# Optimization experiments

Measured on AMD Instinct MI355X. Metric: run time of the kernel, lower is better.

Reference implementation:

```python
import jax, jax.numpy as jnp
import numpy as np

BS, T, F, H, YIN = 32, 64, 32, 256, 10


def setup_inputs() -> dict:
    key = jax.random.key(0)
    ks = jax.random.split(key, 20)
    s = 0.1
    rn = lambda k, shape: jax.random.normal(k, shape, dtype=jnp.float32) * s
    return {
        'Y': jax.random.normal(ks[0], (BS, T, YIN), dtype=jnp.float32),
        'X_p': jax.random.normal(ks[1], (BS, T, F), dtype=jnp.float32),
        'X_n': jax.random.normal(ks[2], (BS, T, F), dtype=jnp.float32),
        # Y-stream LSTM (input 10)
        'Wy': rn(ks[3], (YIN, 4 * H)), 'Uy': rn(ks[4], (H, 4 * H)), 'by': jnp.zeros((4 * H,), jnp.float32),
        # per-feature single-input LSTM banks (F independent LSTMs, input size 1)
        'Wxp': rn(ks[5], (F, 4 * H)), 'Uxp': rn(ks[6], (F, H, 4 * H)), 'bxp': jnp.zeros((F, 4 * H), jnp.float32),
        'Wxn': rn(ks[7], (F, 4 * H)), 'Uxn': rn(ks[8], (F, H, 4 * H)), 'bxn': jnp.zeros((F, 4 * H), jnp.float32),
        # MI-LSTM: main stream gates (i,f,g,o), aux streams (gate, candidate) each
        'Wm': rn(ks[9], (H, 4 * H)), 'Um': rn(ks[10], (H, 4 * H)), 'bm': jnp.zeros((4 * H,), jnp.float32),
        'Wpa': rn(ks[11], (H, 2 * H)), 'Upa': rn(ks[12], (H, 2 * H)), 'bpa': jnp.zeros((2 * H,), jnp.float32),
        'Wna': rn(ks[13], (H, 2 * H)), 'Una': rn(ks[14], (H, 2 * H)), 'bna': jnp.zeros((2 * H,), jnp.float32),
        'Wa': rn(ks[15], (H, H)), 'ba': jnp.zeros((H,), jnp.float32),
        # temporal attention + output head
        'Watt': rn(ks[16], (H, H)), 'batt': jnp.zeros((H,), jnp.float32), 'vatt': rn(ks[17], (H,)),
        'Wlin': rn(ks[18], (H, 1)), 'blin': jnp.zeros((1,), jnp.float32),
    }


def _lstm(x, W, U, b):
    # standard LSTM; x: [bs,T,in] -> hidden sequence [bs,T,H]
    xg = jnp.einsum('bti,ig->btg', x, W) + b  # precompute input projections
    bs, h = x.shape[0], U.shape[0]

    def step(carry, g_t):
        hh, cc = carry
        g = g_t + hh @ U
        i, f, gg, o = jnp.split(g, 4, axis=-1)
        i, f, o = jax.nn.sigmoid(i), jax.nn.sigmoid(f), jax.nn.sigmoid(o)
        cc = f * cc + i * jnp.tanh(gg)
        hh = o * jnp.tanh(cc)
        return (hh, cc), hh

    init = (jnp.zeros((bs, h), x.dtype), jnp.zeros((bs, h), x.dtype))
    _, hs = jax.lax.scan(step, init, jnp.swapaxes(xg, 0, 1))
    return jnp.swapaxes(hs, 0, 1)


def _feature_lstms(x, W, U, b):
    # F independent input-size-1 LSTMs batched into one scan; returns the mean
    # over features of their hidden sequences (= torch.mean(torch.stack(...),0)).
    # x: [bs,T,F], W: [F,4H], U: [F,H,4H], b: [F,4H] -> [bs,T,H]
    xg = x[..., None] * W + b  # [bs,T,F,4H]
    bs, f, h = x.shape[0], W.shape[0], U.shape[1]

    def step(carry, g_t):
        hh, cc = carry  # [bs,F,H]
        g = g_t + jnp.einsum('bfh,fhg->bfg', hh, U)
        i, fg, gg, o = jnp.split(g, 4, axis=-1)
        i, fg, o = jax.nn.sigmoid(i), jax.nn.sigmoid(fg), jax.nn.sigmoid(o)
        cc = fg * cc + i * jnp.tanh(gg)
        hh = o * jnp.tanh(cc)
        return (hh, cc), jnp.mean(hh, axis=1)  # mean over feature-LSTMs

    init = (jnp.zeros((bs, f, h), x.dtype), jnp.zeros((bs, f, h), x.dtype))
    _, hs = jax.lax.scan(step, init, jnp.swapaxes(xg, 0, 1))
    return jnp.swapaxes(hs, 0, 1)


def _milstm(y, p, n, Wm, Um, bm, Wpa, Upa, bpa, Wna, Una, bna, Wa, ba):
    # Multi-input LSTM: main stream y with full i/f/g/o gates; aux streams p,n
    # contribute gated candidates; cell-state attention mixes the 3 candidates.
    yg = jnp.einsum('bth,hg->btg', y, Wm) + bm
    pg = jnp.einsum('bth,hg->btg', p, Wpa) + bpa
    ng = jnp.einsum('bth,hg->btg', n, Wna) + bna
    bs, h = y.shape[0], Um.shape[0]

    def step(carry, gs):
        hh, cc = carry
        yg_t, pg_t, ng_t = gs
        g = yg_t + hh @ Um
        i, f, gy, o = jnp.split(g, 4, axis=-1)
        i, f, o = jax.nn.sigmoid(i), jax.nn.sigmoid(f), jax.nn.sigmoid(o)
        gp = pg_t + hh @ Upa
        ip, cp = jnp.split(gp, 2, axis=-1)
        gn = ng_t + hh @ Una
        inn, cn = jnp.split(gn, 2, axis=-1)
        l = jnp.stack([i * jnp.tanh(gy),
                       jax.nn.sigmoid(ip) * jnp.tanh(cp),
                       jax.nn.sigmoid(inn) * jnp.tanh(cn)], axis=1)  # [bs,3,H]
        att = jnp.tanh(cc @ Wa + ba)  # [bs,H]
        alpha = jax.nn.softmax(jnp.einsum('bkh,bh->bk', l, att), axis=-1)
        ltilde = jnp.einsum('bk,bkh->bh', alpha, l)
        cc = f * cc + ltilde
        hh = o * jnp.tanh(cc)
        return (hh, cc), hh

    init = (jnp.zeros((bs, h), y.dtype), jnp.zeros((bs, h), y.dtype))
    xs = (jnp.swapaxes(yg, 0, 1), jnp.swapaxes(pg, 0, 1), jnp.swapaxes(ng, 0, 1))
    _, hs = jax.lax.scan(step, init, xs)
    return jnp.swapaxes(hs, 0, 1)


def reference(Y, X_p, X_n, Wy, Uy, by, Wxp, Uxp, bxp, Wxn, Uxn, bxn,
              Wm, Um, bm, Wpa, Upa, bpa, Wna, Una, bna, Wa, ba,
              Watt, batt, vatt, Wlin, blin):
    Yh = _lstm(Y, Wy, Uy, by)                      # Y_tilde_hidden [bs,T,H]
    Ph = _feature_lstms(X_p, Wxp, Uxp, bxp)        # P_tilde [bs,T,H]
    Nh = _feature_lstms(X_n, Wxn, Uxn, bxn)        # N_tilde [bs,T,H]
    Hm = _milstm(Yh, Ph, Nh, Wm, Um, bm, Wpa, Upa, bpa, Wna, Una, bna, Wa, ba)
    # temporal additive attention
    s = jnp.einsum('bth,h->bt', jnp.tanh(jnp.einsum('bth,hg->btg', Hm, Watt) + batt), vatt)
    alpha = jax.nn.softmax(s, axis=-1)
    ytilde = jnp.einsum('bt,bth->bh', alpha, Hm)
    return jax.nn.relu(ytilde @ Wlin + blin)       # [bs,1]
```

## Files before the change

kernel.cpp:

```cpp
#include <hip/hip_runtime.h>
#include <math.h>

#define BS 32
#define T 64
#define F 32
#define H 256
#define G4 1024
#define YIN 10

typedef _Float16 f16;
typedef _Float16 f16x8 __attribute__((ext_vector_type(8)));
typedef float f32x4 __attribute__((ext_vector_type(4)));

__device__ __forceinline__ float sigm(float x) { return 1.f / (1.f + expf(-x)); }

__global__ __launch_bounds__(512) void k_prep_u(
    const float* __restrict__ Uxp, const float* __restrict__ Uxn,
    const float* __restrict__ Uy, f16* __restrict__ Uf)
{
  const int slot = blockIdx.x;
  const float* src = (slot < 32) ? (Uxp + (size_t)slot * 262144)
                   : (slot < 64) ? (Uxn + (size_t)(slot - 32) * 262144)
                   : Uy;
  f16* dst = Uf + (size_t)slot * 262144;
  const int lane = threadIdx.x & 63;
  const int kt   = threadIdx.x >> 6;
  const int cl = lane & 15, lq = lane >> 4;
  for (int w = 0; w < 8; ++w)
    for (int nt = 0; nt < 8; ++nt) {
      const int g   = nt >> 1;
      const int col = g * 256 + w * 32 + (nt & 1) * 16 + cl;
      const int k0  = kt * 32 + lq * 8;
      f16x8 v;
      #pragma unroll
      for (int e = 0; e < 8; ++e) v[e] = (f16)src[(size_t)(k0 + e) * G4 + col];
      *(f16x8*)(dst + ((size_t)((w * 8 + nt) * 8 + kt) * 64 + lane) * 8) = v;
    }
}

__global__ __launch_bounds__(1024) void k_prep_w(
    const float* __restrict__ Um, const float* __restrict__ Upa,
    const float* __restrict__ Una, const float* __restrict__ Wa,
    f16* __restrict__ Umh, f16* __restrict__ Uph, f16* __restrict__ Unh,
    f16* __restrict__ Wah)
{
  const int i = blockIdx.x * 1024 + threadIdx.x;
  Umh[i] = (f16)Um[i];
  if (i < 131072) { Uph[i] = (f16)Upa[i]; Unh[i] = (f16)Una[i]; }
  if (i < 65536)  Wah[i] = (f16)Wa[i];
}

__global__ __launch_bounds__(1024) void k_prep_yg0(
    const float* __restrict__ Y, const float* __restrict__ Wy,
    const float* __restrict__ by, float* __restrict__ yg0)
{
  const int col = threadIdx.x;
  const int r0  = blockIdx.x * 16;
  float wv[YIN];
  #pragma unroll
  for (int i = 0; i < YIN; ++i) wv[i] = Wy[i * G4 + col];
  const float bv = by[col];
  for (int r = r0; r < r0 + 16; ++r) {
    float a = bv;
    #pragma unroll
    for (int i = 0; i < YIN; ++i) a += Y[r * YIN + i] * wv[i];
    yg0[(size_t)r * G4 + col] = a;
  }
}

__global__ __launch_bounds__(512, 1) void k_scan(
    const float* __restrict__ Xp, const float* __restrict__ Xn,
    const float* __restrict__ Wxp, const float* __restrict__ bxp,
    const float* __restrict__ Wxn, const float* __restrict__ bxn,
    const f16*  __restrict__ Uf,  const float* __restrict__ yg0,
    float* __restrict__ Yh, float* __restrict__ Ph, float* __restrict__ Nh)
{
  __shared__ __align__(16) f16 hfrag[8 * 64 * 8];
  const int tid = threadIdx.x;
  const int w = tid >> 6, l = tid & 63;
  const int cl = l & 15, lq = l >> 4;
  const int bid = blockIdx.x;
  const bool isY = (bid >= 128);
  int s = 0, f = 0, bh, slot;
  if (isY) { bh = bid & 1; slot = 64; }
  else { s = bid >> 6; f = (bid >> 1) & 31; bh = bid & 1; slot = s * 32 + f; }

  f16x8 U[8][8];
  {
    const f16* ub = Uf + (size_t)slot * 262144 + (size_t)w * 32768 + (size_t)l * 8;
    #pragma unroll
    for (int nt = 0; nt < 8; ++nt)
      #pragma unroll
      for (int kt = 0; kt < 8; ++kt)
        U[nt][kt] = *(const f16x8*)(ub + (nt * 8 + kt) * 512);
  }

  float Wc[4][2], Bc[4][2];
  const float* Xsrc = nullptr;
  if (!isY) {
    const float* Wf = (s ? Wxn : Wxp) + (size_t)f * G4;
    const float* bf = (s ? bxn : bxp) + (size_t)f * G4;
    #pragma unroll
    for (int g = 0; g < 4; ++g)
      #pragma unroll
      for (int q = 0; q < 2; ++q) {
        const int col = g * 256 + w * 32 + q * 16 + cl;
        Wc[g][q] = Wf[col]; Bc[g][q] = bf[col];
      }
    Xsrc = s ? Xn : Xp;
  }
  float* Acc = s ? Nh : Ph;

  float c[2][4];
  #pragma unroll
  for (int q = 0; q < 2; ++q)
    #pragma unroll
    for (int j = 0; j < 4; ++j) c[q][j] = 0.f;

  *(uint4*)(hfrag + tid * 8) = uint4{0, 0, 0, 0};
  __syncthreads();

  for (int t = 0; t < T; ++t) {
    f16x8 a8[8];
    #pragma unroll
    for (int kt = 0; kt < 8; ++kt)
      a8[kt] = *(const f16x8*)(hfrag + kt * 512 + l * 8);

    f32x4 acc[8];
    #pragma unroll
    for (int nt = 0; nt < 8; ++nt) acc[nt] = f32x4{0.f, 0.f, 0.f, 0.f};
    #pragma unroll
    for (int kt = 0; kt < 8; ++kt)
      #pragma unroll
      for (int nt = 0; nt < 8; ++nt)
        acc[nt] = __builtin_amdgcn_mfma_f32_16x16x32_f16(a8[kt], U[nt][kt], acc[nt], 0, 0, 0);

    float xin[4];
    if (!isY) {
      #pragma unroll
      for (int j = 0; j < 4; ++j)
        xin[j] = Xsrc[((size_t)(bh * 16 + lq * 4 + j) * T + t) * F + f];
    }
    __syncthreads();

    #pragma unroll
    for (int q = 0; q < 2; ++q) {
      const int ncol = w * 32 + q * 16 + cl;
      #pragma unroll
      for (int j = 0; j < 4; ++j) {
        const int b = bh * 16 + lq * 4 + j;
        float ip, fp, gp, op;
        if (isY) {
          const float* yrow = yg0 + ((size_t)b * T + t) * G4;
          ip = acc[0 + q][j] + yrow[0 * 256 + ncol];
          fp = acc[2 + q][j] + yrow[1 * 256 + ncol];
          gp = acc[4 + q][j] + yrow[2 * 256 + ncol];
          op = acc[6 + q][j] + yrow[3 * 256 + ncol];
        } else {
          ip = acc[0 + q][j] + xin[j] * Wc[0][q] + Bc[0][q];
          fp = acc[2 + q][j] + xin[j] * Wc[1][q] + Bc[1][q];
          gp = acc[4 + q][j] + xin[j] * Wc[2][q] + Bc[2][q];
          op = acc[6 + q][j] + xin[j] * Wc[3][q] + Bc[3][q];
        }
        const float ig = sigm(ip), fg = sigm(fp), gy = tanhf(gp), og = sigm(op);
        c[q][j] = fg * c[q][j] + ig * gy;
        const float h = og * tanhf(c[q][j]);
        const int dlane = (lq * 4 + j) + (q * 2 + (cl >> 3)) * 16;
        hfrag[w * 512 + dlane * 8 + (cl & 7)] = (f16)h;
        const size_t oidx = ((size_t)b * T + t) * H + ncol;
        if (isY) Yh[oidx] = h;
        else atomicAdd(&Acc[oidx], h * 0.03125f);
      }
    }
    __syncthreads();
  }
}

__global__ __launch_bounds__(1024) void k_xg(
    const float* __restrict__ Yh, const float* __restrict__ Ph, const float* __restrict__ Nh,
    const float* __restrict__ Wm, const float* __restrict__ bm,
    const float* __restrict__ Wpa, const float* __restrict__ bpa,
    const float* __restrict__ Wna, const float* __restrict__ bna,
    float* __restrict__ yg, float* __restrict__ pg, float* __restrict__ ng)
{
  __shared__ __align__(16) float A[8][768];
  const int tid = threadIdx.x;
  const int ro  = blockIdx.x * 8;

  for (int idx = tid; idx < 8 * 768; idx += 1024) {
    const int r = idx / 768, cc = idx % 768;
    const int row = ro + r;
    float v;
    if (cc < 256)      v = Yh[(size_t)row * H + cc];
    else if (cc < 512) v = Ph[(size_t)row * H + (cc - 256)];
    else               v = Nh[(size_t)row * H + (cc - 512)];
    A[r][cc] = v;
  }
  __syncthreads();

  float acc[8];
  #pragma unroll
  for (int r = 0; r < 8; ++r) acc[r] = bm[tid];
  for (int k = 0; k < H; k += 4) {
    const float w0 = Wm[(k + 0) * G4 + tid];
    const float w1 = Wm[(k + 1) * G4 + tid];
    const float w2 = Wm[(k + 2) * G4 + tid];
    const float w3 = Wm[(k + 3) * G4 + tid];
    #pragma unroll
    for (int r = 0; r < 8; ++r) {
      const float4 av = *(const float4*)&A[r][k];
      acc[r] += w0 * av.x + w1 * av.y + w2 * av.z + w3 * av.w;
    }
  }
  #pragma unroll
  for (int r = 0; r < 8; ++r) yg[(size_t)(ro + r) * G4 + tid] = acc[r];

  const int col = tid & 511;
  const float* Wx = (tid < 512) ? Wpa : Wna;
  const float* bx = (tid < 512) ? bpa : bna;
  float* outp     = (tid < 512) ? pg : ng;
  const int aoff  = (tid < 512) ? 256 : 512;
  #pragma unroll
  for (int r = 0; r < 8; ++r) acc[r] = bx[col];
  for (int k = 0; k < H; k += 4) {
    const float w0 = Wx[(k + 0) * 512 + col];
    const float w1 = Wx[(k + 1) * 512 + col];
    const float w2 = Wx[(k + 2) * 512 + col];
    const float w3 = Wx[(k + 3) * 512 + col];
    #pragma unroll
    for (int r = 0; r < 8; ++r) {
      const float4 av = *(const float4*)&A[r][aoff + k];
      acc[r] += w0 * av.x + w1 * av.y + w2 * av.z + w3 * av.w;
    }
  }
  #pragma unroll
  for (int r = 0; r < 8; ++r) outp[(size_t)(ro + r) * 512 + col] = acc[r];
}

__global__ __launch_bounds__(1024) void k_mi(
    const float* __restrict__ yg, const float* __restrict__ pg, const float* __restrict__ ng,
    const f16* __restrict__ Um, const f16* __restrict__ Upa, const f16* __restrict__ Una,
    const f16* __restrict__ Wa, const float* __restrict__ ba,
    float* __restrict__ Hm)
{
  __shared__ __align__(16) float h_lds[H];
  __shared__ __align__(16) float c_lds[H];
  __shared__ float g_lds[G4];
  __shared__ float ga_lds[G4];
  __shared__ float att_lds[H];
  __shared__ float red[3][4];
  const int tid = threadIdx.x;
  const int b   = blockIdx.x;

  if (tid < H) { h_lds[tid] = 0.f; c_lds[tid] = 0.f; }
  __syncthreads();

  for (int t = 0; t < T; ++t) {
    const size_t row = (size_t)b * T + t;

    float gacc = yg[row * G4 + tid];
    for (int k = 0; k < H; k += 4) {
      const float4 hv = *(const float4*)&h_lds[k];
      gacc += (float)Um[(k + 0) * G4 + tid] * hv.x + (float)Um[(k + 1) * G4 + tid] * hv.y
            + (float)Um[(k + 2) * G4 + tid] * hv.z + (float)Um[(k + 3) * G4 + tid] * hv.w;
    }

    const int acol = tid & 511;
    const f16* Ux = (tid < 512) ? Upa : Una;
    float aacc = (tid < 512) ? pg[row * 512 + acol] : ng[row * 512 + acol];
    for (int k = 0; k < H; k += 4) {
      const float4 hv = *(const float4*)&h_lds[k];
      aacc += (float)Ux[(k + 0) * 512 + acol] * hv.x + (float)Ux[(k + 1) * 512 + acol] * hv.y
            + (float)Ux[(k + 2) * 512 + acol] * hv.z + (float)Ux[(k + 3) * 512 + acol] * hv.w;
    }

    float attv = 0.f;
    if (tid < H) {
      attv = ba[tid];
      for (int k = 0; k < H; k += 4) {
        const float4 cv = *(const float4*)&c_lds[k];
        attv += (float)Wa[(k + 0) * H + tid] * cv.x + (float)Wa[(k + 1) * H + tid] * cv.y
              + (float)Wa[(k + 2) * H + tid] * cv.z + (float)Wa[(k + 3) * H + tid] * cv.w;
      }
      attv = tanhf(attv);
    }

    g_lds[tid]  = gacc;
    ga_lds[tid] = aacc;
    if (tid < H) att_lds[tid] = attv;
    __syncthreads();

    float l0 = 0.f, l1 = 0.f, l2 = 0.f, fg = 0.f, og = 0.f;
    if (tid < H) {
      const int n = tid;
      const float ig = sigm(g_lds[n]);
      fg = sigm(g_lds[H + n]);
      const float gy = tanhf(g_lds[2 * H + n]);
      og = sigm(g_lds[3 * H + n]);
      l0 = ig * gy;
      l1 = sigm(ga_lds[n])         * tanhf(ga_lds[H + n]);
      l2 = sigm(ga_lds[2 * H + n]) * tanhf(ga_lds[3 * H + n]);
      const float a = att_lds[n];
      float v0 = l0 * a, v1 = l1 * a, v2 = l2 * a;
      for (int off = 32; off; off >>= 1) {
        v0 += __shfl_down(v0, off);
        v1 += __shfl_down(v1, off);
        v2 += __shfl_down(v2, off);
      }
      if ((tid & 63) == 0) {
        red[0][tid >> 6] = v0; red[1][tid >> 6] = v1; red[2][tid >> 6] = v2;
      }
    }
    __syncthreads();

    if (tid < H) {
      const int n = tid;
      const float s0 = red[0][0] + red[0][1] + red[0][2] + red[0][3];
      const float s1 = red[1][0] + red[1][1] + red[1][2] + red[1][3];
      const float s2 = red[2][0] + red[2][1] + red[2][2] + red[2][3];
      const float m  = fmaxf(s0, fmaxf(s1, s2));
      const float e0 = expf(s0 - m), e1 = expf(s1 - m), e2 = expf(s2 - m);
      const float inv = 1.f / (e0 + e1 + e2);
      const float lt  = (e0 * l0 + e1 * l1 + e2 * l2) * inv;
      const float cc  = fg * c_lds[n] + lt;
      const float h   = og * tanhf(cc);
      c_lds[n] = cc;
      h_lds[n] = h;
      Hm[row * H + n] = h;
    }
    __syncthreads();
  }
}

__global__ __launch_bounds__(256) void k_att(
    const float* __restrict__ Hm, const float* __restrict__ Watt, const float* __restrict__ batt,
    const float* __restrict__ vatt, const float* __restrict__ Wlin, const float* __restrict__ blin,
    float* __restrict__ out)
{
  __shared__ __align__(16) float hm8[8][H];
  __shared__ float vred[8][4];
  __shared__ float s_lds[T];
  __shared__ float alpha_lds[T];
  __shared__ float red4[4];
  const int n = threadIdx.x;
  const int b = blockIdx.x;
  const float bn = batt[n], vn = vatt[n];

  for (int t0 = 0; t0 < T; t0 += 8) {
    __syncthreads();
    #pragma unroll
    for (int r = 0; r < 8; ++r) hm8[r][n] = Hm[((size_t)b * T + t0 + r) * H + n];
    __syncthreads();
    float acc[8];
    #pragma unroll
    for (int r = 0; r < 8; ++r) acc[r] = bn;
    for (int k = 0; k < H; k += 4) {
      const float w0 = Watt[(k + 0) * H + n];
      const float w1 = Watt[(k + 1) * H + n];
      const float w2 = Watt[(k + 2) * H + n];
      const float w3 = Watt[(k + 3) * H + n];
      #pragma unroll
      for (int r = 0; r < 8; ++r) {
        const float4 hv = *(const float4*)&hm8[r][k];
        acc[r] += w0 * hv.x + w1 * hv.y + w2 * hv.z + w3 * hv.w;
      }
    }
    #pragma unroll
    for (int r = 0; r < 8; ++r) {
      float v = tanhf(acc[r]) * vn;
      for (int off = 32; off; off >>= 1) v += __shfl_down(v, off);
      if ((n & 63) == 0) vred[r][n >> 6] = v;
    }
    __syncthreads();
    if (n < 8) s_lds[t0 + n] = vred[n][0] + vred[n][1] + vred[n][2] + vred[n][3];
  }
  __syncthreads();

  if (n < T) {
    const float sv = s_lds[n];
    float m = sv;
    for (int off = 32; off; off >>= 1) m = fmaxf(m, __shfl_xor(m, off));
    const float e = expf(sv - m);
    float sum = e;
    for (int off = 32; off; off >>= 1) sum += __shfl_xor(sum, off);
    alpha_lds[n] = e / sum;
  }
  __syncthreads();

  float acc = 0.f;
  for (int t = 0; t < T; ++t) acc += alpha_lds[t] * Hm[((size_t)b * T + t) * H + n];
  float p = acc * Wlin[n];
  for (int off = 32; off; off >>= 1) p += __shfl_down(p, off);
  if ((n & 63) == 0) red4[n >> 6] = p;
  __syncthreads();
  if (n == 0) out[b] = fmaxf(red4[0] + red4[1] + red4[2] + red4[3] + blin[0], 0.f);
}

extern "C" void kernel_launch(void* const* d_in, const int* in_sizes, int n_in,
                              void* d_out, int out_size, void* d_ws, size_t ws_size,
                              hipStream_t stream) {
  const float* Yin  = (const float*)d_in[0];
  const float* Xp   = (const float*)d_in[1];
  const float* Xn   = (const float*)d_in[2];
  const float* Wy   = (const float*)d_in[3];
  const float* Uy   = (const float*)d_in[4];
  const float* by   = (const float*)d_in[5];
  const float* Wxp  = (const float*)d_in[6];
  const float* Uxp  = (const float*)d_in[7];
  const float* bxp  = (const float*)d_in[8];
  const float* Wxn  = (const float*)d_in[9];
  const float* Uxn  = (const float*)d_in[10];
  const float* bxn  = (const float*)d_in[11];
  const float* Wm   = (const float*)d_in[12];
  const float* Um   = (const float*)d_in[13];
  const float* bm   = (const float*)d_in[14];
  const float* Wpa  = (const float*)d_in[15];
  const float* Upa  = (const float*)d_in[16];
  const float* bpa  = (const float*)d_in[17];
  const float* Wna  = (const float*)d_in[18];
  const float* Una  = (const float*)d_in[19];
  const float* bna  = (const float*)d_in[20];
  const float* Wa   = (const float*)d_in[21];
  const float* ba   = (const float*)d_in[22];
  const float* Watt = (const float*)d_in[23];
  const float* batt = (const float*)d_in[24];
  const float* vatt = (const float*)d_in[25];
  const float* Wlin = (const float*)d_in[26];
  const float* blin = (const float*)d_in[27];

  float* ws = (float*)d_ws;
  float* Yh  = ws;
  float* Ph  = ws + 524288;
  float* Nh  = ws + 1048576;
  float* Hm  = ws + 1572864;
  float* yg  = ws + 2097152;
  float* pg  = ws + 4194304;
  float* ng  = ws + 5242880;
  float* yg0 = ws + 6291456;
  f16*   Uf  = (f16*)(ws + 8388608);
  f16*   Umh = (f16*)(ws + 16908288);
  f16*   Uph = (f16*)(ws + 17039360);
  f16*   Unh = (f16*)(ws + 17104896);
  f16*   Wah = (f16*)(ws + 17170432);
  float* out = (float*)d_out;

  hipMemsetAsync(Ph, 0, (size_t)2 * 524288 * sizeof(float), stream);

  k_prep_u  <<<65, 512, 0, stream>>>(Uxp, Uxn, Uy, Uf);
  k_prep_w  <<<256, 1024, 0, stream>>>(Um, Upa, Una, Wa, Umh, Uph, Unh, Wah);
  k_prep_yg0<<<128, 1024, 0, stream>>>(Yin, Wy, by, yg0);

  k_scan<<<130, 512, 0, stream>>>(Xp, Xn, Wxp, bxp, Wxn, bxn, Uf, yg0, Yh, Ph, Nh);
  k_xg  <<<256, 1024, 0, stream>>>(Yh, Ph, Nh, Wm, bm, Wpa, bpa, Wna, bna, yg, pg, ng);
  k_mi  <<<32, 1024, 0, stream>>>(yg, pg, ng, Umh, Uph, Unh, Wah, ba, Hm);
  k_att <<<32, 256, 0, stream>>>(Hm, Watt, batt, vatt, Wlin, blin, out);
}
```

Before: 2.216 ms.

## Restructure scan and MI-LSTM kernels around cross-block grid barriers and MFMA

The feature/Y LSTM scan now runs each LSTM as a pair of blocks, each holding half the hidden columns for all 32 batch rows. Hidden state is exchanged through a double-buffered global array, with a spin-wait grid barrier after every step. The MI-LSTM recurrence moves from 32 per-batch blocks doing scalar fp32 matvecs to 16 blocks that split hidden columns and use f16 MFMA with pre-swizzled weights. Its attention softmax reduction goes through a global partial-sum buffer and two grid barriers per step. Activations switch to fast __expf-based sigmoid and tanh, and inputs are pre-transposed for coalesced loads. This adds correctness risk from relying on all blocks being co-resident for the spin barriers, plus per-step barrier latency and reduced f16 precision in the MI-LSTM.

```diff
diff --git a/kernel.cpp b/kernel.cpp
--- a/kernel.cpp
+++ b/kernel.cpp
@@ -1,178 +1,207 @@
 #include <hip/hip_runtime.h>
 #include <math.h>
 
-#define BS 32
 #define T 64
-#define F 32
 #define H 256
-#define G4 1024
-#define YIN 10
 
 typedef _Float16 f16;
 typedef _Float16 f16x8 __attribute__((ext_vector_type(8)));
 typedef float f32x4 __attribute__((ext_vector_type(4)));
 
-__device__ __forceinline__ float sigm(float x) { return 1.f / (1.f + expf(-x)); }
+__device__ __forceinline__ float sigm(float x) { return 1.f / (1.f + __expf(-x)); }
+__device__ __forceinline__ float ftanh(float x) { return 1.f - 2.f / (__expf(2.f * x) + 1.f); }
+
+__device__ __forceinline__ void gridbar(unsigned* bar, unsigned target) {
+  __threadfence();
+  __syncthreads();
+  if (threadIdx.x == 0) {
+    __hip_atomic_fetch_add(bar, 1u, __ATOMIC_ACQ_REL, __HIP_MEMORY_SCOPE_AGENT);
+    while (__hip_atomic_load(bar, __ATOMIC_ACQUIRE, __HIP_MEMORY_SCOPE_AGENT) < target)
+      __builtin_amdgcn_s_sleep(1);
+    __threadfence();
+  }
+  __syncthreads();
+}
 
 __global__ __launch_bounds__(512) void k_prep_u(
     const float* __restrict__ Uxp, const float* __restrict__ Uxn,
-    const float* __restrict__ Uy, f16* __restrict__ Uf)
-{
-  const int slot = blockIdx.x;
-  const float* src = (slot < 32) ? (Uxp + (size_t)slot * 262144)
-                   : (slot < 64) ? (Uxn + (size_t)(slot - 32) * 262144)
+    const float* __restrict__ Uy, f16* __restrict__ Uf2)
+{
+  const int unit = blockIdx.x;
+  const int lstm = unit >> 4, slice = unit & 15;
+  const float* src = (lstm < 32) ? (Uxp + (size_t)lstm * 262144)
+                   : (lstm < 64) ? (Uxn + (size_t)(lstm - 32) * 262144)
                    : Uy;
-  f16* dst = Uf + (size_t)slot * 262144;
-  const int lane = threadIdx.x & 63;
-  const int kt   = threadIdx.x >> 6;
-  const int cl = lane & 15, lq = lane >> 4;
-  for (int w = 0; w < 8; ++w)
-    for (int nt = 0; nt < 8; ++nt) {
-      const int g   = nt >> 1;
-      const int col = g * 256 + w * 32 + (nt & 1) * 16 + cl;
-      const int k0  = kt * 32 + lq * 8;
-      f16x8 v;
-      #pragma unroll
-      for (int e = 0; e < 8; ++e) v[e] = (f16)src[(size_t)(k0 + e) * G4 + col];
-      *(f16x8*)(dst + ((size_t)((w * 8 + nt) * 8 + kt) * 64 + lane) * 8) = v;
-    }
-}
-
-__global__ __launch_bounds__(1024) void k_prep_w(
+  for (int fl = threadIdx.x; fl < 2048; fl += 512) {
+    const int g = fl >> 9, kt = (fl >> 6) & 7, l = fl & 63;
+    const int col = g * 256 + slice * 16 + (l & 15);
+    const int k0 = kt * 32 + (l >> 4) * 8;
+    f16x8 v;
+    #pragma unroll
+    for (int e = 0; e < 8; ++e) v[e] = (f16)src[(size_t)(k0 + e) * 1024 + col];
+    *(f16x8*)(Uf2 + (((size_t)unit * 32 + g * 8 + kt) * 512) + (size_t)l * 8) = v;
+  }
+}
+
+__global__ __launch_bounds__(512) void k_prep_umi(
     const float* __restrict__ Um, const float* __restrict__ Upa,
     const float* __restrict__ Una, const float* __restrict__ Wa,
-    f16* __restrict__ Umh, f16* __restrict__ Uph, f16* __restrict__ Unh,
-    f16* __restrict__ Wah)
-{
-  const int i = blockIdx.x * 1024 + threadIdx.x;
-  Umh[i] = (f16)Um[i];
-  if (i < 131072) { Uph[i] = (f16)Upa[i]; Unh[i] = (f16)Una[i]; }
-  if (i < 65536)  Wah[i] = (f16)Wa[i];
+    f16* __restrict__ Ufmi)
+{
+  const int blk = blockIdx.x / 9, slot = blockIdx.x % 9;
+  const int kt = threadIdx.x >> 6, l = threadIdx.x & 63;
+  const int n = blk * 16 + (l & 15);
+  const int k0 = kt * 32 + (l >> 4) * 8;
+  const float* src; int col, ld;
+  if (slot < 4)      { src = Um;  col = slot * 256 + n;       ld = 1024; }
+  else if (slot < 6) { src = Upa; col = (slot - 4) * 256 + n; ld = 512;  }
+  else if (slot < 8) { src = Una; col = (slot - 6) * 256 + n; ld = 512;  }
+  else               { src = Wa;  col = n;                    ld = 256;  }
+  f16x8 v;
+  #pragma unroll
+  for (int e = 0; e < 8; ++e) v[e] = (f16)src[(size_t)(k0 + e) * ld + col];
+  *(f16x8*)(Ufmi + (((size_t)blk * 9 + slot) * 8 + kt) * 512 + (size_t)l * 8) = v;
+}
+
+__global__ __launch_bounds__(512) void k_prep_x(
+    const float* __restrict__ Xp, const float* __restrict__ Xn, float* __restrict__ Xt)
+{
+  const int s = blockIdx.x >> 5, f = blockIdx.x & 31;
+  const float* X = s ? Xn : Xp;
+  for (int i = threadIdx.x; i < 2048; i += 512) {
+    const int t = i >> 5, b = i & 31;
+    Xt[((size_t)(s * 32 + f) * 64 + t) * 32 + b] = X[((size_t)b * 64 + t) * 32 + f];
+  }
 }
 
 __global__ __launch_bounds__(1024) void k_prep_yg0(
     const float* __restrict__ Y, const float* __restrict__ Wy,
-    const float* __restrict__ by, float* __restrict__ yg0)
-{
-  const int col = threadIdx.x;
-  const int r0  = blockIdx.x * 16;
-  float wv[YIN];
-  #pragma unroll
-  for (int i = 0; i < YIN; ++i) wv[i] = Wy[i * G4 + col];
+    const float* __restrict__ by, float* __restrict__ yg0t)
+{
+  const int t = blockIdx.x, col = threadIdx.x;
+  float wv[10];
+  #pragma unroll
+  for (int i = 0; i < 10; ++i) wv[i] = Wy[i * 1024 + col];
   const float bv = by[col];
-  for (int r = r0; r < r0 + 16; ++r) {
+  for (int b = 0; b < 32; ++b) {
     float a = bv;
     #pragma unroll
-    for (int i = 0; i < YIN; ++i) a += Y[r * YIN + i] * wv[i];
-    yg0[(size_t)r * G4 + col] = a;
-  }
-}
-
-__global__ __launch_bounds__(512, 1) void k_scan(
-    const float* __restrict__ Xp, const float* __restrict__ Xn,
+    for (int i = 0; i < 10; ++i) a += Y[((size_t)b * 64 + t) * 10 + i] * wv[i];
+    yg0t[((size_t)t * 1024 + col) * 32 + b] = a;
+  }
+}
+
+__global__ __launch_bounds__(512, 2) void k_scan(
+    const float* __restrict__ Xt,
     const float* __restrict__ Wxp, const float* __restrict__ bxp,
     const float* __restrict__ Wxn, const float* __restrict__ bxn,
-    const f16*  __restrict__ Uf,  const float* __restrict__ yg0,
-    float* __restrict__ Yh, float* __restrict__ Ph, float* __restrict__ Nh)
-{
-  __shared__ __align__(16) f16 hfrag[8 * 64 * 8];
+    const f16* __restrict__ Uf2, const float* __restrict__ yg0t,
+    f16* __restrict__ hg, float* __restrict__ Yh,
+    float* __restrict__ Ph, float* __restrict__ Nh, unsigned* __restrict__ bars)
+{
+  __shared__ __align__(16) f16 hs[32 * 256];
   const int tid = threadIdx.x;
   const int w = tid >> 6, l = tid & 63;
   const int cl = l & 15, lq = l >> 4;
   const int bid = blockIdx.x;
-  const bool isY = (bid >= 128);
-  int s = 0, f = 0, bh, slot;
-  if (isY) { bh = bid & 1; slot = 64; }
-  else { s = bid >> 6; f = (bid >> 1) & 31; bh = bid & 1; slot = s * 32 + f; }
-
-  f16x8 U[8][8];
+  const int lstm = bid >> 1, half = bid & 1;
+  const int slice = half * 8 + w;
+  const int n = slice * 16 + cl;
+  const bool isY = (lstm == 64);
+  const int s = (lstm >= 32) ? 1 : 0;
+  const int f = lstm & 31;
+
+  f16x8 U[4][8];
   {
-    const f16* ub = Uf + (size_t)slot * 262144 + (size_t)w * 32768 + (size_t)l * 8;
-    #pragma unroll
-    for (int nt = 0; nt < 8; ++nt)
+    const f16* ub = Uf2 + ((size_t)(lstm * 16 + slice) * 32) * 512 + (size_t)l * 8;
+    #pragma unroll
+    for (int g = 0; g < 4; ++g)
       #pragma unroll
       for (int kt = 0; kt < 8; ++kt)
-        U[nt][kt] = *(const f16x8*)(ub + (nt * 8 + kt) * 512);
-  }
-
-  float Wc[4][2], Bc[4][2];
-  const float* Xsrc = nullptr;
+        U[g][kt] = *(const f16x8*)(ub + (size_t)(g * 8 + kt) * 512);
+  }
+
+  float Wc[4], Bc[4];
+  const float* xrow = nullptr;
   if (!isY) {
-    const float* Wf = (s ? Wxn : Wxp) + (size_t)f * G4;
-    const float* bf = (s ? bxn : bxp) + (size_t)f * G4;
-    #pragma unroll
-    for (int g = 0; g < 4; ++g)
-      #pragma unroll
-      for (int q = 0; q < 2; ++q) {
-        const int col = g * 256 + w * 32 + q * 16 + cl;
-        Wc[g][q] = Wf[col]; Bc[g][q] = bf[col];
-      }
-    Xsrc = s ? Xn : Xp;
+    const float* Wf = (s ? Wxn : Wxp) + (size_t)f * 1024;
+    const float* bf = (s ? bxn : bxp) + (size_t)f * 1024;
+    #pragma unroll
+    for (int g = 0; g < 4; ++g) { Wc[g] = Wf[g * 256 + n]; Bc[g] = bf[g * 256 + n]; }
+    xrow = Xt + (size_t)(s * 32 + f) * 64 * 32;
   }
   float* Acc = s ? Nh : Ph;
-
-  float c[2][4];
-  #pragma unroll
-  for (int q = 0; q < 2; ++q)
-    #pragma unroll
-    for (int j = 0; j < 4; ++j) c[q][j] = 0.f;
-
-  *(uint4*)(hfrag + tid * 8) = uint4{0, 0, 0, 0};
-  __syncthreads();
+  unsigned* bar = bars + lstm * 32;
+
+  float c[2][4] = {{0.f, 0.f, 0.f, 0.f}, {0.f, 0.f, 0.f, 0.f}};
 
   for (int t = 0; t < T; ++t) {
-    f16x8 a8[8];
-    #pragma unroll
-    for (int kt = 0; kt < 8; ++kt)
-      a8[kt] = *(const f16x8*)(hfrag + kt * 512 + l * 8);
-
-    f32x4 acc[8];
-    #pragma unroll
-    for (int nt = 0; nt < 8; ++nt) acc[nt] = f32x4{0.f, 0.f, 0.f, 0.f};
-    #pragma unroll
-    for (int kt = 0; kt < 8; ++kt)
-      #pragma unroll
-      for (int nt = 0; nt < 8; ++nt)
-        acc[nt] = __builtin_amdgcn_mfma_f32_16x16x32_f16(a8[kt], U[nt][kt], acc[nt], 0, 0, 0);
-
-    float xin[4];
-    if (!isY) {
-      #pragma unroll
-      for (int j = 0; j < 4; ++j)
-        xin[j] = Xsrc[((size_t)(bh * 16 + lq * 4 + j) * T + t) * F + f];
+    {
+      const uint4* src = (const uint4*)(hg + ((size_t)(t & 1) * 65 + lstm) * 8192);
+      #pragma unroll
+      for (int i = 0; i < 2; ++i) {
+        const int idx4 = tid * 2 + i;
+        const uint4 v = src[idx4];
+        const int byte = idx4 * 16;
+        const int b = byte >> 9, kb = byte & 511;
+        *(uint4*)((char*)hs + b * 512 + (kb ^ ((b & 7) << 4))) = v;
+      }
     }
     __syncthreads();
 
-    #pragma unroll
-    for (int q = 0; q < 2; ++q) {
-      const int ncol = w * 32 + q * 16 + cl;
+    f32x4 acc[4][2];
+    #pragma unroll
+    for (int g = 0; g < 4; ++g) { acc[g][0] = f32x4{0,0,0,0}; acc[g][1] = f32x4{0,0,0,0}; }
+    #pragma unroll
+    for (int mt = 0; mt < 2; ++mt) {
+      f16x8 a8[8];
+      const int row = 16 * mt + cl;
+      #pragma unroll
+      for (int kt = 0; kt < 8; ++kt)
+        a8[kt] = *(const f16x8*)((char*)hs + row * 512 + ((kt * 64 + lq * 16) ^ ((cl & 7) << 4)));
+      #pragma unroll
+      for (int kt = 0; kt < 8; ++kt)
+        #pragma unroll
+        for (int g = 0; g < 4; ++g)
+          acc[g][mt] = __builtin_amdgcn_mfma_f32_16x16x32_f16(a8[kt], U[g][kt], acc[g][mt], 0, 0, 0);
+    }
+
+    f16* dst = hg + ((size_t)((t + 1) & 1) * 65 + lstm) * 8192;
+    #pragma unroll
+    for (int mt = 0; mt < 2; ++mt) {
+      float4 xv; float4 yv[4];
+      if (!isY) xv = *(const float4*)(xrow + t * 32 + 16 * mt + lq * 4);
+      else {
+        #pragma unroll
+        for (int g = 0; g < 4; ++g)
+          yv[g] = *(const float4*)(yg0t + ((size_t)t * 1024 + g * 256 + n) * 32 + 16 * mt + lq * 4);
+      }
+      const float* xp = (const float*)&xv;
       #pragma unroll
       for (int j = 0; j < 4; ++j) {
-        const int b = bh * 16 + lq * 4 + j;
-        float ip, fp, gp, op;
-        if (isY) {
-          const float* yrow = yg0 + ((size_t)b * T + t) * G4;
-          ip = acc[0 + q][j] + yrow[0 * 256 + ncol];
-          fp = acc[2 + q][j] + yrow[1 * 256 + ncol];
-          gp = acc[4 + q][j] + yrow[2 * 256 + ncol];
-          op = acc[6 + q][j] + yrow[3 * 256 + ncol];
+        const int b = 16 * mt + lq * 4 + j;
+        float p0, p1, p2, p3;
+        if (!isY) {
+          const float x = xp[j];
+          p0 = acc[0][mt][j] + x * Wc[0] + Bc[0];
+          p1 = acc[1][mt][j] + x * Wc[1] + Bc[1];
+          p2 = acc[2][mt][j] + x * Wc[2] + Bc[2];
+          p3 = acc[3][mt][j] + x * Wc[3] + Bc[3];
         } else {
-          ip = acc[0 + q][j] + xin[j] * Wc[0][q] + Bc[0][q];
-          fp = acc[2 + q][j] + xin[j] * Wc[1][q] + Bc[1][q];
-          gp = acc[4 + q][j] + xin[j] * Wc[2][q] + Bc[2][q];
-          op = acc[6 + q][j] + xin[j] * Wc[3][q] + Bc[3][q];
+          p0 = acc[0][mt][j] + ((const float*)&yv[0])[j];
+          p1 = acc[1][mt][j] + ((const float*)&yv[1])[j];
+          p2 = acc[2][mt][j] + ((const float*)&yv[2])[j];
+          p3 = acc[3][mt][j] + ((const float*)&yv[3])[j];
         }
-        const float ig = sigm(ip), fg = sigm(fp), gy = tanhf(gp), og = sigm(op);
-        c[q][j] = fg * c[q][j] + ig * gy;
-        const float h = og * tanhf(c[q][j]);
-        const int dlane = (lq * 4 + j) + (q * 2 + (cl >> 3)) * 16;
-        hfrag[w * 512 + dlane * 8 + (cl & 7)] = (f16)h;
-        const size_t oidx = ((size_t)b * T + t) * H + ncol;
-        if (isY) Yh[oidx] = h;
-        else atomicAdd(&Acc[oidx], h * 0.03125f);
-      }
-    }
-    __syncthreads();
+        const float ig = sigm(p0), fg = sigm(p1), gy = ftanh(p2), og = sigm(p3);
+        c[mt][j] = fg * c[mt][j] + ig * gy;
+        const float h = og * ftanh(c[mt][j]);
+        dst[b * 256 + n] = (f16)h;
+        if (!isY) atomicAdd(&Acc[((size_t)b * T + t) * H + n], h * 0.03125f);
+        else Yh[((size_t)b * T + t) * H + n] = h;
+      }
+    }
+    if (t < T - 1) gridbar(bar, 2u * (unsigned)(t + 1));
   }
 }
 
@@ -202,10 +231,10 @@
   #pragma unroll
   for (int r = 0; r < 8; ++r) acc[r] = bm[tid];
   for (int k = 0; k < H; k += 4) {
-    const float w0 = Wm[(k + 0) * G4 + tid];
-    const float w1 = Wm[(k + 1) * G4 + tid];
-    const float w2 = Wm[(k + 2) * G4 + tid];
-    const float w3 = Wm[(k + 3) * G4 + tid];
+    const float w0 = Wm[(k + 0) * 1024 + tid];
+    const float w1 = Wm[(k + 1) * 1024 + tid];
+    const float w2 = Wm[(k + 2) * 1024 + tid];
+    const float w3 = Wm[(k + 3) * 1024 + tid];
     #pragma unroll
     for (int r = 0; r < 8; ++r) {
       const float4 av = *(const float4*)&A[r][k];
@@ -213,7 +242,7 @@
     }
   }
   #pragma unroll
-  for (int r = 0; r < 8; ++r) yg[(size_t)(ro + r) * G4 + tid] = acc[r];
+  for (int r = 0; r < 8; ++r) yg[(size_t)(ro + r) * 1024 + tid] = acc[r];
 
   const int col = tid & 511;
   const float* Wx = (tid < 512) ? Wpa : Wna;
@@ -237,98 +266,103 @@
   for (int r = 0; r < 8; ++r) outp[(size_t)(ro + r) * 512 + col] = acc[r];
 }
 
-__global__ __launch_bounds__(1024) void k_mi(
+__global__ __launch_bounds__(576) void k_mi(
     const float* __restrict__ yg, const float* __restrict__ pg, const float* __restrict__ ng,
-    const f16* __restrict__ Um, const f16* __restrict__ Upa, const f16* __restrict__ Una,
-    const f16* __restrict__ Wa, const float* __restrict__ ba,
-    float* __restrict__ Hm)
-{
-  __shared__ __align__(16) float h_lds[H];
-  __shared__ __align__(16) float c_lds[H];
-  __shared__ float g_lds[G4];
-  __shared__ float ga_lds[G4];
-  __shared__ float att_lds[H];
-  __shared__ float red[3][4];
+    const f16* __restrict__ Ufmi, const float* __restrict__ ba,
+    f16* __restrict__ Hh, f16* __restrict__ Hc, float* __restrict__ Spart,
+    unsigned* __restrict__ bar, float* __restrict__ Hm)
+{
+  __shared__ float g_lds[9][32][16];
   const int tid = threadIdx.x;
-  const int b   = blockIdx.x;
-
-  if (tid < H) { h_lds[tid] = 0.f; c_lds[tid] = 0.f; }
-  __syncthreads();
+  const int w = tid >> 6, l = tid & 63;
+  const int cl = l & 15, lq = l >> 4;
+  const int blk = blockIdx.x;
+
+  f16x8 U[8];
+  #pragma unroll
+  for (int kt = 0; kt < 8; ++kt)
+    U[kt] = *(const f16x8*)(Ufmi + (((size_t)blk * 9 + w) * 8 + kt) * 512 + (size_t)l * 8);
+
+  const int b2 = tid >> 4, nl = tid & 15;
+  const int n2 = blk * 16 + nl;
+  const float bav = ba[n2];
+  float creg = 0.f;
+  unsigned cnt = 0;
 
   for (int t = 0; t < T; ++t) {
-    const size_t row = (size_t)b * T + t;
-
-    float gacc = yg[row * G4 + tid];
-    for (int k = 0; k < H; k += 4) {
-      const float4 hv = *(const float4*)&h_lds[k];
-      gacc += (float)Um[(k + 0) * G4 + tid] * hv.x + (float)Um[(k + 1) * G4 + tid] * hv.y
-            + (float)Um[(k + 2) * G4 + tid] * hv.z + (float)Um[(k + 3) * G4 + tid] * hv.w;
-    }
-
-    const int acol = tid & 511;
-    const f16* Ux = (tid < 512) ? Upa : Una;
-    float aacc = (tid < 512) ? pg[row * 512 + acol] : ng[row * 512 + acol];
-    for (int k = 0; k < H; k += 4) {
-      const float4 hv = *(const float4*)&h_lds[k];
-      aacc += (float)Ux[(k + 0) * 512 + acol] * hv.x + (float)Ux[(k + 1) * 512 + acol] * hv.y
-            + (float)Ux[(k + 2) * 512 + acol] * hv.z + (float)Ux[(k + 3) * 512 + acol] * hv.w;
-    }
-
-    float attv = 0.f;
-    if (tid < H) {
-      attv = ba[tid];
-      for (int k = 0; k < H; k += 4) {
-        const float4 cv = *(const float4*)&c_lds[k];
-        attv += (float)Wa[(k + 0) * H + tid] * cv.x + (float)Wa[(k + 1) * H + tid] * cv.y
-              + (float)Wa[(k + 2) * H + tid] * cv.z + (float)Wa[(k + 3) * H + tid] * cv.w;
-      }
-      attv = tanhf(attv);
-    }
-
-    g_lds[tid]  = gacc;
-    ga_lds[tid] = aacc;
-    if (tid < H) att_lds[tid] = attv;
+    float pre[8];
+    if (tid < 512) {
+      const size_t row = (size_t)b2 * T + t;
+      #pragma unroll
+      for (int g = 0; g < 4; ++g) pre[g] = yg[row * 1024 + g * 256 + n2];
+      pre[4] = pg[row * 512 + n2];       pre[5] = pg[row * 512 + 256 + n2];
+      pre[6] = ng[row * 512 + n2];       pre[7] = ng[row * 512 + 256 + n2];
+    }
+    const f16* asrc = (w == 8) ? Hc : Hh;
+    f32x4 acc[2] = {f32x4{0,0,0,0}, f32x4{0,0,0,0}};
+    #pragma unroll
+    for (int mt = 0; mt < 2; ++mt) {
+      f16x8 a8[8];
+      #pragma unroll
+      for (int kt = 0; kt < 8; ++kt)
+        a8[kt] = *(const f16x8*)(asrc + (16 * mt + cl) * 256 + kt * 32 + lq * 8);
+      #pragma unroll
+      for (int kt = 0; kt < 8; ++kt)
+        acc[mt] = __builtin_amdgcn_mfma_f32_16x16x32_f16(a8[kt], U[kt], acc[mt], 0, 0, 0);
+    }
+    #pragma unroll
+    for (int mt = 0; mt < 2; ++mt)
+      #pragma unroll
+      for (int j = 0; j < 4; ++j)
+        g_lds[w][lq * 4 + j + 16 * mt][cl] = acc[mt][j];
     __syncthreads();
 
     float l0 = 0.f, l1 = 0.f, l2 = 0.f, fg = 0.f, og = 0.f;
-    if (tid < H) {
-      const int n = tid;
-      const float ig = sigm(g_lds[n]);
-      fg = sigm(g_lds[H + n]);
-      const float gy = tanhf(g_lds[2 * H + n]);
-      og = sigm(g_lds[3 * H + n]);
-      l0 = ig * gy;
-      l1 = sigm(ga_lds[n])         * tanhf(ga_lds[H + n]);
-      l2 = sigm(ga_lds[2 * H + n]) * tanhf(ga_lds[3 * H + n]);
-      const float a = att_lds[n];
-      float v0 = l0 * a, v1 = l1 * a, v2 = l2 * a;
-      for (int off = 32; off; off >>= 1) {
-        v0 += __shfl_down(v0, off);
-        v1 += __shfl_down(v1, off);
-        v2 += __shfl_down(v2, off);
-      }
-      if ((tid & 63) == 0) {
-        red[0][tid >> 6] = v0; red[1][tid >> 6] = v1; red[2][tid >> 6] = v2;
-      }
-    }
-    __syncthreads();
-
-    if (tid < H) {
-      const int n = tid;
-      const float s0 = red[0][0] + red[0][1] + red[0][2] + red[0][3];
-      const float s1 = red[1][0] + red[1][1] + red[1][2] + red[1][3];
-      const float s2 = red[2][0] + red[2][1] + red[2][2] + red[2][3];
-      const float m  = fmaxf(s0, fmaxf(s1, s2));
-      const float e0 = expf(s0 - m), e1 = expf(s1 - m), e2 = expf(s2 - m);
-      const float inv = 1.f / (e0 + e1 + e2);
-      const float lt  = (e0 * l0 + e1 * l1 + e2 * l2) * inv;
-      const float cc  = fg * c_lds[n] + lt;
-      const float h   = og * tanhf(cc);
-      c_lds[n] = cc;
-      h_lds[n] = h;
-      Hm[row * H + n] = h;
-    }
-    __syncthreads();
+    if (tid < 512) {
+      const float gi = sigm(g_lds[0][b2][nl] + pre[0]);
+      fg             = sigm(g_lds[1][b2][nl] + pre[1]);
+      const float gy = ftanh(g_lds[2][b2][nl] + pre[2]);
+      og             = sigm(g_lds[3][b2][nl] + pre[3]);
+      const float ip = sigm(g_lds[4][b2][nl] + pre[4]);
+      const float cp = ftanh(g_lds[5][b2][nl] + pre[5]);
+      const float in = sigm(g_lds[6][b2][nl] + pre[6]);
+      const float cn = ftanh(g_lds[7][b2][nl] + pre[7]);
+      const float att = ftanh(g_lds[8][b2][nl] + bav);
+      l0 = gi * gy; l1 = ip * cp; l2 = in * cn;
+      float v0 = l0 * att, v1 = l1 * att, v2 = l2 * att;
+      #pragma unroll
+      for (int off = 1; off < 16; off <<= 1) {
+        v0 += __shfl_xor(v0, off);
+        v1 += __shfl_xor(v1, off);
+        v2 += __shfl_xor(v2, off);
+      }
+      if (nl == 0) {
+        float* sp = Spart + ((size_t)t * 32 + b2) * 48 + blk;
+        sp[0] = v0; sp[16] = v1; sp[32] = v2;
+      }
+    }
+    ++cnt; gridbar(bar, 16u * cnt);
+    if (tid < 512) {
+      float sv = 0.f;
+      if (nl < 3) {
+        const float* sp = Spart + ((size_t)t * 32 + b2) * 48 + nl * 16;
+        #pragma unroll
+        for (int q = 0; q < 16; ++q) sv += sp[q];
+      }
+      const int base = l & 0x30;
+      const float s0 = __shfl(sv, base | 0);
+      const float s1 = __shfl(sv, base | 1);
+      const float s2 = __shfl(sv, base | 2);
+      const float m = fmaxf(s0, fmaxf(s1, s2));
+      const float e0 = __expf(s0 - m), e1 = __expf(s1 - m), e2 = __expf(s2 - m);
+      const float lt = (e0 * l0 + e1 * l1 + e2 * l2) / (e0 + e1 + e2);
+      creg = fg * creg + lt;
+      const float h = og * ftanh(creg);
+      Hh[b2 * 256 + n2] = (f16)h;
+      Hc[b2 * 256 + n2] = (f16)creg;
+      Hm[((size_t)b2 * T + t) * H + n2] = h;
+    }
+    if (t < T - 1) { ++cnt; gridbar(bar, 16u * cnt); }
   }
 }
 
@@ -429,29 +463,37 @@
   const float* blin = (const float*)d_in[27];
 
   float* ws = (float*)d_ws;
-  float* Yh  = ws;
-  float* Ph  = ws + 524288;
-  float* Nh  = ws + 1048576;
-  float* Hm  = ws + 1572864;
-  float* yg  = ws + 2097152;
-  float* pg  = ws + 4194304;
-  float* ng  = ws + 5242880;
-  float* yg0 = ws + 6291456;
-  f16*   Uf  = (f16*)(ws + 8388608);
-  f16*   Umh = (f16*)(ws + 16908288);
-  f16*   Uph = (f16*)(ws + 17039360);
-  f16*   Unh = (f16*)(ws + 17104896);
-  f16*   Wah = (f16*)(ws + 17170432);
-  float* out = (float*)d_out;
-
-  hipMemsetAsync(Ph, 0, (size_t)2 * 524288 * sizeof(float), stream);
-
-  k_prep_u  <<<65, 512, 0, stream>>>(Uxp, Uxn, Uy, Uf);
-  k_prep_w  <<<256, 1024, 0, stream>>>(Um, Upa, Una, Wa, Umh, Uph, Unh, Wah);
-  k_prep_yg0<<<128, 1024, 0, stream>>>(Yin, Wy, by, yg0);
-
-  k_scan<<<130, 512, 0, stream>>>(Xp, Xn, Wxp, bxp, Wxn, bxn, Uf, yg0, Yh, Ph, Nh);
+  float*    Yh    = ws;
+  float*    Ph    = ws + 524288;
+  float*    Nh    = ws + 1048576;
+  float*    Hm    = ws + 1572864;
+  float*    yg    = ws + 2097152;
+  float*    pg    = ws + 4194304;
+  float*    ng    = ws + 5242880;
+  float*    yg0t  = ws + 6291456;
+  float*    Xt    = ws + 8388608;
+  f16*      Uf2   = (f16*)(ws + 8519680);
+  f16*      Ufmi  = (f16*)(ws + 17039360);
+  f16*      hg    = (f16*)(ws + 17334272);
+  f16*      Hh    = (f16*)(ws + 17866752);
+  f16*      Hc    = (f16*)(ws + 17870848);
+  float*    Spart = ws + 17874944;
+  unsigned* bars  = (unsigned*)(ws + 17973248);
+  float*    out   = (float*)d_out;
+
+  hipMemsetAsync(Ph,   0, (size_t)2 * 524288 * sizeof(float), stream);
+  hipMemsetAsync(hg,   0, (size_t)1064960 * sizeof(f16), stream);
+  hipMemsetAsync(Hh,   0, (size_t)2 * 8192 * sizeof(f16), stream);
+  hipMemsetAsync(bars, 0, (size_t)2112 * sizeof(unsigned), stream);
+
+  k_prep_u   <<<1040, 512, 0, stream>>>(Uxp, Uxn, Uy, Uf2);
+  k_prep_umi <<<144, 512, 0, stream>>>(Um, Upa, Una, Wa, Ufmi);
+  k_prep_x   <<<64, 512, 0, stream>>>(Xp, Xn, Xt);
+  k_prep_yg0 <<<64, 1024, 0, stream>>>(Yin, Wy, by, yg0t);
+
+  k_scan<<<130, 512, 0, stream>>>(Xt, Wxp, bxp, Wxn, bxn, Uf2, yg0t,
+                                  hg, Yh, Ph, Nh, bars);
   k_xg  <<<256, 1024, 0, stream>>>(Yh, Ph, Nh, Wm, bm, Wpa, bpa, Wna, bna, yg, pg, ng);
-  k_mi  <<<32, 1024, 0, stream>>>(yg, pg, ng, Umh, Uph, Unh, Wah, ba, Hm);
+  k_mi  <<<16, 576, 0, stream>>>(yg, pg, ng, Ufmi, ba, Hh, Hc, Spart, bars + 2080, Hm);
   k_att <<<32, 256, 0, stream>>>(Hm, Watt, batt, vatt, Wlin, blin, out);
 }
```

Result: slower. 3.614 ms (+63.1%).
